# Optimization experiments

Measured on AMD Instinct MI355X. Metric: run time of the kernel, lower is better.

Reference implementation:

```python
import jax, jax.numpy as jnp
import numpy as np

TEMPERATURE = 0.5
B, D = 4096, 256

def setup_inputs() -> dict:
    key = jax.random.key(0)
    k1, k2 = jax.random.split(key)
    z_i = jax.random.normal(k1, (B, D), dtype=jnp.float32)
    z_j = jax.random.normal(k2, (B, D), dtype=jnp.float32)
    return {"z_i": z_i, "z_j": z_j}

def reference(z_i, z_j):
    # NT-Xent loss (SimCLR). Cosine similarity of L2-normalized rows == dot product.
    b = z_i.shape[0]
    n = 2 * b
    zi = z_i / jnp.linalg.norm(z_i, axis=1, keepdims=True)
    zj = z_j / jnp.linalg.norm(z_j, axis=1, keepdims=True)
    z = jnp.concatenate([zi, zj], axis=0)            # [N, D]
    sim = jnp.matmul(z, z.T)                          # [N, N] cosine-sim matrix
    # positives: sim(i, i+b) and sim(i+b, i)
    pos = jnp.concatenate([jnp.diagonal(sim, offset=b), jnp.diagonal(sim, offset=-b)])  # [N]
    logits = sim / TEMPERATURE
    # Cross-entropy with the positive as the target class over {pos} U negatives.
    # The candidate set per row is all j != i (the positive j = partner(i) is included,
    # only the self-similarity diagonal is excluded) -> mask diagonal with -inf.
    neg_inf = jnp.asarray(-jnp.inf, dtype=logits.dtype)
    masked = jnp.where(jnp.eye(n, dtype=bool), neg_inf, logits)
    lse = jax.nn.logsumexp(masked, axis=1)            # [N]
    loss = jnp.sum(lse - pos / TEMPERATURE) / n
    return loss
```

## Files before the change

### kernel.cpp

```cpp
#include <hip/hip_runtime.h>
#include <hip/hip_bf16.h>


constexpr int BB = 4096;
constexpr int NN = 8192;
constexpr int DD = 256;
constexpr int RT = 256;
constexpr int CC = 512;
constexpr int NRT = NN / RT;
constexpr int NCH = NN / CC;
constexpr int CSTEPS = CC / 32;

typedef _Float16 half4v __attribute__((ext_vector_type(4)));
typedef _Float16 half8v __attribute__((ext_vector_type(8)));
typedef float floatx16 __attribute__((ext_vector_type(16)));

__global__ __launch_bounds__(256) void nt_normalize(
    const float* __restrict__ zi, const float* __restrict__ zj,
    _Float16* __restrict__ Z, float* __restrict__ posPartial)
{
    const int lane = threadIdx.x & 63;
    const int wave = threadIdx.x >> 6;
    const int i = blockIdx.x * 4 + wave;

    const float4 a = ((const float4*)(zi + (size_t)i * DD))[lane];
    const float4 b = ((const float4*)(zj + (size_t)i * DD))[lane];

    float ssi = a.x*a.x + a.y*a.y + a.z*a.z + a.w*a.w;
    float ssj = b.x*b.x + b.y*b.y + b.z*b.z + b.w*b.w;
    float dd  = a.x*b.x + a.y*b.y + a.z*b.z + a.w*b.w;
#pragma unroll
    for (int off = 32; off > 0; off >>= 1) {
        ssi += __shfl_xor(ssi, off);
        ssj += __shfl_xor(ssj, off);
        dd  += __shfl_xor(dd,  off);
    }
    const float invi = rsqrtf(ssi);
    const float invj = rsqrtf(ssj);

    half4v ha, hb;
    ha.x = (_Float16)(a.x * invi); ha.y = (_Float16)(a.y * invi);
    ha.z = (_Float16)(a.z * invi); ha.w = (_Float16)(a.w * invi);
    hb.x = (_Float16)(b.x * invj); hb.y = (_Float16)(b.y * invj);
    hb.z = (_Float16)(b.z * invj); hb.w = (_Float16)(b.w * invj);

    ((half4v*)(Z + (size_t)i * DD))[lane]        = ha;
    ((half4v*)(Z + (size_t)(BB + i) * DD))[lane] = hb;

    __shared__ float ps[4];
    if (lane == 0) ps[wave] = dd * invi * invj;
    __syncthreads();
    if (threadIdx.x == 0)
        posPartial[blockIdx.x] = ps[0] + ps[1] + ps[2] + ps[3];
}

__global__ __launch_bounds__(256, 2) void nt_simexp(
    const _Float16* __restrict__ Z, float* __restrict__ rowsum)
{
    __shared__ _Float16 lds[32 * DD];

    const int bid = blockIdx.x;
    const int rt = bid & (NRT - 1);
    const int ch = bid >> 5;
    const int tid = threadIdx.x;
    const int wave = tid >> 6;
    const int lane = tid & 63;
    const int lm = lane & 31;
    const int lh = lane >> 5;

    const int rbase = rt * RT + wave * 64;

    half8v bfrag[2][16];
#pragma unroll
    for (int b = 0; b < 2; ++b) {
        const _Float16* rowp = Z + (size_t)(rbase + b * 32 + lm) * DD + lh * 8;
#pragma unroll
        for (int s = 0; s < 16; ++s)
            bfrag[b][s] = *(const half8v*)(rowp + s * 16);
    }

    float ea0 = 0.f, ea1 = 0.f;
    const int cchunk = ch * CC;
    const bool blockdiag = (ch == (rt >> 1));
    const float KEXP = 2.0f * 1.44269504088896340736f;

    for (int cs = 0; cs < CSTEPS; ++cs) {
        const int cbase = cchunk + cs * 32;

        __syncthreads();
#pragma unroll
        for (int it = 0; it < 4; ++it) {
            const int g = tid + it * 256;
            const int c = g >> 5;
            const int kc = g & 31;
            half8v gv = *(const half8v*)(Z + (size_t)(cbase + c) * DD + kc * 8);
            *(half8v*)(&lds[c * DD + (kc ^ (c & 7)) * 8]) = gv;
        }
        __syncthreads();

        floatx16 c0, c1;
#pragma unroll
        for (int r = 0; r < 16; ++r) { c0[r] = 0.f; c1[r] = 0.f; }

#pragma unroll
        for (int s = 0; s < 16; ++s) {
            const int phys = (2 * s + lh) ^ (lm & 7);
            half8v af = *(const half8v*)(&lds[lm * DD + phys * 8]);
            c0 = __builtin_amdgcn_mfma_f32_32x32x16_f16(af, bfrag[0][s], c0, 0, 0, 0);
            c1 = __builtin_amdgcn_mfma_f32_32x32x16_f16(af, bfrag[1][s], c1, 0, 0, 0);
        }

        const bool m0 = blockdiag && (cbase == rbase);
        const bool m1 = blockdiag && (cbase == rbase + 32);
        if (!(m0 | m1)) {
#pragma unroll
            for (int r = 0; r < 16; ++r) {
                ea0 += __builtin_amdgcn_exp2f(c0[r] * KEXP);
                ea1 += __builtin_amdgcn_exp2f(c1[r] * KEXP);
            }
        } else {
#pragma unroll
            for (int r = 0; r < 16; ++r) {
                const int mrow = (r & 3) + 8 * (r >> 2) + 4 * lh;
                float e0 = __builtin_amdgcn_exp2f(c0[r] * KEXP);
                float e1 = __builtin_amdgcn_exp2f(c1[r] * KEXP);
                if (m0 && (mrow == lm)) e0 = 0.f;
                if (m1 && (mrow == lm)) e1 = 0.f;
                ea0 += e0; ea1 += e1;
            }
        }
    }

    ea0 += __shfl_xor(ea0, 32);
    ea1 += __shfl_xor(ea1, 32);
    if (lane < 32) {
        atomicAdd(&rowsum[rbase + lm], ea0);
        atomicAdd(&rowsum[rbase + 32 + lm], ea1);
    }
}

__global__ __launch_bounds__(256) void nt_finalize(
    const float* __restrict__ rowsum, const float* __restrict__ posPartial,
    float* __restrict__ out)
{
    const int tid = threadIdx.x;
    float acc = 0.f;
#pragma unroll
    for (int it = 0; it < NN / 256; ++it)
        acc += __builtin_amdgcn_logf(rowsum[tid + it * 256]);
    float pacc = 0.f;
#pragma unroll
    for (int it = 0; it < 4; ++it)
        pacc += posPartial[tid + it * 256];

#pragma unroll
    for (int off = 32; off > 0; off >>= 1) {
        acc  += __shfl_xor(acc,  off);
        pacc += __shfl_xor(pacc, off);
    }
    __shared__ float sa[4], sp[4];
    const int wave = tid >> 6;
    if ((tid & 63) == 0) { sa[wave] = acc; sp[wave] = pacc; }
    __syncthreads();
    if (tid == 0) {
        const float lntot = (sa[0] + sa[1] + sa[2] + sa[3]) * 0.6931471805599453f;
        const float ptot  = sp[0] + sp[1] + sp[2] + sp[3];
        out[0] = (lntot - 4.0f * ptot) * (1.0f / (float)NN);
    }
}

extern "C" void kernel_launch(void* const* d_in, const int* in_sizes, int n_in,
                              void* d_out, int out_size, void* d_ws, size_t ws_size,
                              hipStream_t stream) {
    const float* zi = (const float*)d_in[0];
    const float* zj = (const float*)d_in[1];
    float* out = (float*)d_out;

    _Float16* Z = (_Float16*)d_ws;
    float* rowsum = (float*)((char*)d_ws + (size_t)NN * DD * 2);
    float* posPartial = rowsum + NN;

    hipMemsetAsync(rowsum, 0, NN * sizeof(float), stream);
    nt_normalize<<<BB / 4, 256, 0, stream>>>(zi, zj, Z, posPartial);
    nt_simexp<<<NRT * NCH, 256, 0, stream>>>((const _Float16*)Z, rowsum);
    nt_finalize<<<1, 256, 0, stream>>>(rowsum, posPartial, out);
}
```

Measured before the change: 100.1 us.

## Prefetch next column tile into registers during MFMA; fold rowsum zeroing into normalize

The similarity kernel now issues the global loads for the next 32-column tile into registers before computing on the current LDS tile, and writes them to LDS after a barrier at the end of the step. This is meant to hide global load latency behind the MFMA and exp work. The separate memset of rowsum is removed, and the first 32 blocks of the normalize kernel zero it instead, saving one launch. It keeps two barriers per step and adds register pressure from the prefetch buffer, which could affect occupancy under the two-blocks-per-CU launch bound.

Result: faster. 96.96 us (-3.1%).

```diff
diff --git a/kernel.cpp b/kernel.cpp
--- a/kernel.cpp
+++ b/kernel.cpp
@@ -17,11 +17,14 @@
 
 __global__ __launch_bounds__(256) void nt_normalize(
     const float* __restrict__ zi, const float* __restrict__ zj,
-    _Float16* __restrict__ Z, float* __restrict__ posPartial)
+    _Float16* __restrict__ Z, float* __restrict__ posPartial,
+    float* __restrict__ rowsum)
 {
     const int lane = threadIdx.x & 63;
     const int wave = threadIdx.x >> 6;
     const int i = blockIdx.x * 4 + wave;
+
+    if (blockIdx.x < 32) rowsum[blockIdx.x * 256 + threadIdx.x] = 0.f;
 
     const float4 a = ((const float4*)(zi + (size_t)i * DD))[lane];
     const float4 b = ((const float4*)(zj + (size_t)i * DD))[lane];
@@ -79,24 +82,38 @@
             bfrag[b][s] = *(const half8v*)(rowp + s * 16);
     }
 
+    const int g_c0 = tid >> 5;
+    const int g_kc = tid & 31;
+
+    half8v pre[4];
+    auto loadTile = [&](int cbase) {
+#pragma unroll
+        for (int it = 0; it < 4; ++it) {
+            const int c = g_c0 + it * 8;
+            pre[it] = *(const half8v*)(Z + (size_t)(cbase + c) * DD + g_kc * 8);
+        }
+    };
+    auto storeTile = [&]() {
+#pragma unroll
+        for (int it = 0; it < 4; ++it) {
+            const int c = g_c0 + it * 8;
+            *(half8v*)(&lds[c * DD + (g_kc ^ (c & 7)) * 8]) = pre[it];
+        }
+    };
+
     float ea0 = 0.f, ea1 = 0.f;
     const int cchunk = ch * CC;
     const bool blockdiag = (ch == (rt >> 1));
     const float KEXP = 2.0f * 1.44269504088896340736f;
 
+    loadTile(cchunk);
+    storeTile();
+
     for (int cs = 0; cs < CSTEPS; ++cs) {
         const int cbase = cchunk + cs * 32;
 
         __syncthreads();
-#pragma unroll
-        for (int it = 0; it < 4; ++it) {
-            const int g = tid + it * 256;
-            const int c = g >> 5;
-            const int kc = g & 31;
-            half8v gv = *(const half8v*)(Z + (size_t)(cbase + c) * DD + kc * 8);
-            *(half8v*)(&lds[c * DD + (kc ^ (c & 7)) * 8]) = gv;
-        }
-        __syncthreads();
+        if (cs + 1 < CSTEPS) loadTile(cchunk + (cs + 1) * 32);
 
         floatx16 c0, c1;
 #pragma unroll
@@ -129,6 +146,9 @@
                 ea0 += e0; ea1 += e1;
             }
         }
+
+        __syncthreads();
+        if (cs + 1 < CSTEPS) storeTile();
     }
 
     ea0 += __shfl_xor(ea0, 32);
@@ -180,8 +200,7 @@
     float* rowsum = (float*)((char*)d_ws + (size_t)NN * DD * 2);
     float* posPartial = rowsum + NN;
 
-    hipMemsetAsync(rowsum, 0, NN * sizeof(float), stream);
-    nt_normalize<<<BB / 4, 256, 0, stream>>>(zi, zj, Z, posPartial);
+    nt_normalize<<<BB / 4, 256, 0, stream>>>(zi, zj, Z, posPartial, rowsum);
     nt_simexp<<<NRT * NCH, 256, 0, stream>>>((const _Float16*)Z, rowsum);
     nt_finalize<<<1, 256, 0, stream>>>(rowsum, posPartial, out);
 }
```

## Stream A fragments from global, fold exp scale into normalization, drop memset

Applied to the files above, without the earlier changes.

Replaces the per-step LDS staging of the 32-row column tile (with two barriers) by direct global loads of the A fragment, software-prefetched one step ahead. The constant 2*log2(e) is folded into the normalized vectors by scaling each by sqrt of it, so the exp2 needs no multiply, and the positive term is rescaled back. The rowsum memset is moved into the normalize kernel, and the exp accumulators are split to shorten dependency chains. This relies on L2/L1 hits for the repeated column loads, and the scaled fp16 values carry slightly different rounding.

After: 129.5 us. +29.4%, slower.

```diff
diff --git a/kernel.cpp b/kernel.cpp
--- a/kernel.cpp
+++ b/kernel.cpp
@@ -15,13 +15,18 @@
 typedef _Float16 half8v __attribute__((ext_vector_type(8)));
 typedef float floatx16 __attribute__((ext_vector_type(16)));
 
+#define SQK 1.69864414f
+
 __global__ __launch_bounds__(256) void nt_normalize(
     const float* __restrict__ zi, const float* __restrict__ zj,
-    _Float16* __restrict__ Z, float* __restrict__ posPartial)
+    _Float16* __restrict__ Z, float* __restrict__ posPartial,
+    float* __restrict__ rowsum)
 {
     const int lane = threadIdx.x & 63;
     const int wave = threadIdx.x >> 6;
     const int i = blockIdx.x * 4 + wave;
+
+    if (blockIdx.x < 32) rowsum[blockIdx.x * 256 + threadIdx.x] = 0.f;
 
     const float4 a = ((const float4*)(zi + (size_t)i * DD))[lane];
     const float4 b = ((const float4*)(zj + (size_t)i * DD))[lane];
@@ -35,8 +40,8 @@
         ssj += __shfl_xor(ssj, off);
         dd  += __shfl_xor(dd,  off);
     }
-    const float invi = rsqrtf(ssi);
-    const float invj = rsqrtf(ssj);
+    const float invi = rsqrtf(ssi) * SQK;
+    const float invj = rsqrtf(ssj) * SQK;
 
     half4v ha, hb;
     ha.x = (_Float16)(a.x * invi); ha.y = (_Float16)(a.y * invi);
@@ -48,7 +53,7 @@
     ((half4v*)(Z + (size_t)(BB + i) * DD))[lane] = hb;
 
     __shared__ float ps[4];
-    if (lane == 0) ps[wave] = dd * invi * invj;
+    if (lane == 0) ps[wave] = dd * invi * invj * (1.0f / (SQK * SQK));
     __syncthreads();
     if (threadIdx.x == 0)
         posPartial[blockIdx.x] = ps[0] + ps[1] + ps[2] + ps[3];
@@ -57,8 +62,6 @@
 __global__ __launch_bounds__(256, 2) void nt_simexp(
     const _Float16* __restrict__ Z, float* __restrict__ rowsum)
 {
-    __shared__ _Float16 lds[32 * DD];
-
     const int bid = blockIdx.x;
     const int rt = bid & (NRT - 1);
     const int ch = bid >> 5;
@@ -79,24 +82,16 @@
             bfrag[b][s] = *(const half8v*)(rowp + s * 16);
     }
 
-    float ea0 = 0.f, ea1 = 0.f;
+    float ea0 = 0.f, ea1 = 0.f, eb0 = 0.f, eb1 = 0.f;
     const int cchunk = ch * CC;
     const bool blockdiag = (ch == (rt >> 1));
-    const float KEXP = 2.0f * 1.44269504088896340736f;
+
+    const _Float16* ap = Z + (size_t)(cchunk + lm) * DD + lh * 8;
+    half8v a_next = *(const half8v*)ap;
 
     for (int cs = 0; cs < CSTEPS; ++cs) {
         const int cbase = cchunk + cs * 32;
-
-        __syncthreads();
-#pragma unroll
-        for (int it = 0; it < 4; ++it) {
-            const int g = tid + it * 256;
-            const int c = g >> 5;
-            const int kc = g & 31;
-            half8v gv = *(const half8v*)(Z + (size_t)(cbase + c) * DD + kc * 8);
-            *(half8v*)(&lds[c * DD + (kc ^ (c & 7)) * 8]) = gv;
-        }
-        __syncthreads();
+        const _Float16* p = ap + (size_t)cs * 32 * DD;
 
         floatx16 c0, c1;
 #pragma unroll
@@ -104,8 +99,10 @@
 
 #pragma unroll
         for (int s = 0; s < 16; ++s) {
-            const int phys = (2 * s + lh) ^ (lm & 7);
-            half8v af = *(const half8v*)(&lds[lm * DD + phys * 8]);
+            half8v af = a_next;
+            const _Float16* np = (s < 15) ? (p + (s + 1) * 16)
+                                          : (p + (size_t)32 * DD);
+            a_next = *(const half8v*)np;
             c0 = __builtin_amdgcn_mfma_f32_32x32x16_f16(af, bfrag[0][s], c0, 0, 0, 0);
             c1 = __builtin_amdgcn_mfma_f32_32x32x16_f16(af, bfrag[1][s], c1, 0, 0, 0);
         }
@@ -114,23 +111,27 @@
         const bool m1 = blockdiag && (cbase == rbase + 32);
         if (!(m0 | m1)) {
 #pragma unroll
-            for (int r = 0; r < 16; ++r) {
-                ea0 += __builtin_amdgcn_exp2f(c0[r] * KEXP);
-                ea1 += __builtin_amdgcn_exp2f(c1[r] * KEXP);
+            for (int r = 0; r < 16; r += 2) {
+                ea0 += __builtin_amdgcn_exp2f(c0[r]);
+                eb0 += __builtin_amdgcn_exp2f(c0[r + 1]);
+                ea1 += __builtin_amdgcn_exp2f(c1[r]);
+                eb1 += __builtin_amdgcn_exp2f(c1[r + 1]);
             }
         } else {
 #pragma unroll
             for (int r = 0; r < 16; ++r) {
                 const int mrow = (r & 3) + 8 * (r >> 2) + 4 * lh;
-                float e0 = __builtin_amdgcn_exp2f(c0[r] * KEXP);
-                float e1 = __builtin_amdgcn_exp2f(c1[r] * KEXP);
+                float e0 = __builtin_amdgcn_exp2f(c0[r]);
+                float e1 = __builtin_amdgcn_exp2f(c1[r]);
                 if (m0 && (mrow == lm)) e0 = 0.f;
                 if (m1 && (mrow == lm)) e1 = 0.f;
-                ea0 += e0; ea1 += e1;
+                if (r & 1) { eb0 += e0; eb1 += e1; }
+                else       { ea0 += e0; ea1 += e1; }
             }
         }
     }
 
+    ea0 += eb0; ea1 += eb1;
     ea0 += __shfl_xor(ea0, 32);
     ea1 += __shfl_xor(ea1, 32);
     if (lane < 32) {
@@ -180,8 +181,7 @@
     float* rowsum = (float*)((char*)d_ws + (size_t)NN * DD * 2);
     float* posPartial = rowsum + NN;
 
-    hipMemsetAsync(rowsum, 0, NN * sizeof(float), stream);
-    nt_normalize<<<BB / 4, 256, 0, stream>>>(zi, zj, Z, posPartial);
+    nt_normalize<<<BB / 4, 256, 0, stream>>>(zi, zj, Z, posPartial, rowsum);
     nt_simexp<<<NRT * NCH, 256, 0, stream>>>((const _Float16*)Z, rowsum);
     nt_finalize<<<1, 256, 0, stream>>>(rowsum, posPartial, out);
 }
```
